# Performance work log

Hardware: AMD Instinct MI355X
Metric: run time of the kernel (lower is better)

Reference implementation:

```python
import jax, jax.numpy as jnp
import numpy as np

B, S, L, H, C = 16, 2048, 256, 768, 512

def setup_inputs() -> dict:
    key = jax.random.key(0)
    ks = jax.random.split(key, 9)
    sc = 1.0 / np.sqrt(H)
    return {
        "input_hidden_states": jax.random.normal(ks[0], (B, S, H), jnp.float32),
        "label_hidden_states": jax.random.normal(ks[1], (L, H), jnp.float32),
        "Wi": jax.random.normal(ks[2], (C, H), jnp.float32) * sc,
        "bi": jnp.zeros((C,), jnp.float32),
        "Wl": jax.random.normal(ks[3], (C, H), jnp.float32) * sc,
        "bl": jnp.zeros((C,), jnp.float32),
        "Wia": jax.random.normal(ks[4], (C, H), jnp.float32) * sc,
        "bia": jnp.zeros((C,), jnp.float32),
        "Wla": jax.random.normal(ks[5], (C, H), jnp.float32) * sc,
        "bla": jnp.zeros((C,), jnp.float32),
        "context": jax.random.uniform(ks[6], (C,), jnp.float32),
        "Wp": jax.random.normal(ks[7], (H, C), jnp.float32) * (1.0 / np.sqrt(C)),
    }

def reference(input_hidden_states, label_hidden_states, Wi, bi, Wl, bl,
              Wia, bia, Wla, bla, context, Wp):
    # Dropout is identity in eval mode.
    x = input_hidden_states            # [B,S,H]
    lab = label_hidden_states          # [L,H] (original repeats over batch; math is identical)
    input_trans = jax.nn.sigmoid(jnp.einsum('bsh,ch->bsc', x, Wi) + bi)      # [B,S,C]
    label_trans = jax.nn.sigmoid(lab @ Wl.T + bl)                            # [L,C]
    input_attn = jax.nn.sigmoid(jnp.einsum('bsh,ch->bsc', x, Wia) + bia)    # [B,S,C]
    label_attn = jax.nn.sigmoid(lab @ Wla.T + bla)                          # [L,C]
    # attn logits: (context * input_attn) @ label_attn^T  -> [B,S,L]
    logits = jnp.einsum('bsc,lc->bsl', input_attn * context, label_attn)
    attn = jax.nn.softmax(logits, axis=-1)                                   # [B,S,L]
    # trilinear reduction: sum_{s,l} input_trans[b,s,c] * attn[b,s,l] * label_trans[l,c]
    weighted = jnp.einsum('bsl,lc->bsc', attn, label_trans)                  # [B,S,C]
    fusion = jnp.sum(input_trans * weighted, axis=1)                         # [B,C]
    return fusion @ Wp.T                                                     # [B,H]
```

## Files before the change

### kernel.cpp

```cpp
#include <hip/hip_runtime.h>

#define H_DIM 768
#define C_DIM 512
#define L_DIM 256
#define S_DIM 2048
#define B_DIM 16

#define IA_STRIDE 520
#define ATTN_STRIDE 264
#define XP_STRIDE 776

typedef __attribute__((ext_vector_type(8))) short short8;
typedef __attribute__((ext_vector_type(4))) float f32x4;
typedef __attribute__((ext_vector_type(2))) __fp16 half2v;

#define MFMA_F16(a, b, c) __builtin_amdgcn_mfma_f32_16x16x32_f16((a), (b), (c), 0, 0, 0)

__device__ __forceinline__ unsigned short f2h(float f) {
    _Float16 h = (_Float16)f;
    return __builtin_bit_cast(unsigned short, h);
}
__device__ __forceinline__ float h2f(unsigned short u) {
    _Float16 h = __builtin_bit_cast(_Float16, u);
    return (float)h;
}
__device__ __forceinline__ float sigmoid_f(float x) { return 1.0f / (1.0f + __expf(-x)); }

__device__ __forceinline__ short8 cvt8(const float* p) {
    const float4* q = (const float4*)(const void*)p;
    float4 u = q[0], v = q[1];
    half2v h0 = __builtin_amdgcn_cvt_pkrtz(u.x, u.y);
    half2v h1 = __builtin_amdgcn_cvt_pkrtz(u.z, u.w);
    half2v h2 = __builtin_amdgcn_cvt_pkrtz(v.x, v.y);
    half2v h3 = __builtin_amdgcn_cvt_pkrtz(v.z, v.w);
    int4 pk = { __builtin_bit_cast(int, h0), __builtin_bit_cast(int, h1),
                __builtin_bit_cast(int, h2), __builtin_bit_cast(int, h3) };
    return __builtin_bit_cast(short8, pk);
}


__global__ __launch_bounds__(256) void prep_all(
    const float* __restrict__ x,
    const float* __restrict__ Wi, const float* __restrict__ Wia,
    const float* __restrict__ lab,
    const float* __restrict__ Wl,  const float* __restrict__ bl,
    const float* __restrict__ Wla, const float* __restrict__ bla,
    const float* __restrict__ ctx,
    unsigned short* __restrict__ x_f,
    unsigned short* __restrict__ Wi_f, unsigned short* __restrict__ Wia_f,
    unsigned short* __restrict__ la_f, unsigned short* __restrict__ lt_f,
    float* __restrict__ fusion)
{
    __shared__ unsigned short tile[16 * XP_STRIDE];
    const int t   = threadIdx.x;
    const int bid = blockIdx.x;

    if (bid == 0) {
        float4 z = {0.f, 0.f, 0.f, 0.f};
        float4* fp = (float4*)(void*)fusion;
#pragma unroll
        for (int i = 0; i < 8; ++i) fp[i * 256 + t] = z;
        return;
    }

    if (bid < 65) {
        const int lbid = bid - 1;
        const int wave = t >> 6;
        const int lane = t & 63;
        const int quad = lane >> 4;
        const int c16  = lane & 15;
        const int ct2  = lbid & 7;
        const int mh   = lbid >> 3;
        const int ct   = ct2 * 4 + wave;
        const int n0   = ct * 16;
        const int l0   = mh * 32;

        const f32x4 z4 = {0.f, 0.f, 0.f, 0.f};
        f32x4 a1[2], a2[2];
#pragma unroll
        for (int mt = 0; mt < 2; ++mt) { a1[mt] = z4; a2[mt] = z4; }

        const float* lb   = lab + (size_t)(l0 + c16) * H_DIM + quad * 8;
        const float* wlp  = Wl  + (size_t)(n0 + c16) * H_DIM + quad * 8;
        const float* wlap = Wla + (size_t)(n0 + c16) * H_DIM + quad * 8;
        for (int kt = 0; kt < 24; ++kt) {
            short8 b1 = cvt8(wlp + kt * 32);
            short8 b2 = cvt8(wlap + kt * 32);
#pragma unroll
            for (int mt = 0; mt < 2; ++mt) {
                short8 a = cvt8(lb + mt * 16 * H_DIM + kt * 32);
                a1[mt] = MFMA_F16(a, b1, a1[mt]);
                a2[mt] = MFMA_F16(a, b2, a2[mt]);
            }
        }
        const int c = n0 + c16;
        const float blv = bl[c], blav = bla[c], cv = ctx[c];
#pragma unroll
        for (int mt = 0; mt < 2; ++mt)
#pragma unroll
            for (int r = 0; r < 4; ++r) {
                const int l = l0 + mt * 16 + quad * 4 + r;
                const float ltv = sigmoid_f(a1[mt][r] + blv);
                const float lav = sigmoid_f(a2[mt][r] + blav) * cv;
                {
                    const int ctc = c >> 4, ktl = l >> 5;
                    const int frag = ((ctc >> 3) * 8 + ktl) * 8 + (ctc & 7);
                    const int ln = (c & 15) | (((l >> 3) & 3) << 4);
                    lt_f[((size_t)frag * 64 + ln) * 8 + (l & 7)] = f2h(ltv);
                }
                {
                    const int lt = l >> 4, ktc = c >> 5;
                    const int frag = ((lt >> 2) * 16 + ktc) * 4 + (lt & 3);
                    const int ln = (l & 15) | (((c >> 3) & 3) << 4);
                    la_f[((size_t)frag * 64 + ln) * 8 + (c & 7)] = f2h(lav);
                }
            }
        return;
    }

    if (bid < 449) {
        const int tid = (bid - 65) * 256 + t;
        const int m   = tid / 49152;
        const int idx = tid - m * 49152;
        const int ct   = idx / 1536;
        const int rem  = idx - ct * 1536;
        const int kt   = rem >> 6;
        const int lane = rem & 63;
        const int row  = ct * 16 + (lane & 15);
        const int kcol = kt * 32 + (lane >> 4) * 8;
        const float* src = (m == 0 ? Wi : Wia);
        unsigned short* dst = (m == 0 ? Wi_f : Wia_f);
        short8 v = cvt8(src + (size_t)row * H_DIM + kcol);
        const int frag = ((ct >> 3) * 24 + kt) * 8 + (ct & 7);
        *(short8*)(void*)(dst + ((size_t)frag * 64 + lane) * 8) = v;
        return;
    }

    {
        const int mt = bid - 449;
        const float4* src = (const float4*)(const void*)(x + (size_t)mt * 16 * H_DIM);
#pragma unroll
        for (int i = 0; i < 12; ++i) {
            const int id  = i * 256 + t;
            const int row = id / 192;
            const int c4  = id - row * 192;
            float4 v = src[id];
            half2v h0 = __builtin_amdgcn_cvt_pkrtz(v.x, v.y);
            half2v h1 = __builtin_amdgcn_cvt_pkrtz(v.z, v.w);
            uint2 pk = { __builtin_bit_cast(unsigned int, h0),
                         __builtin_bit_cast(unsigned int, h1) };
            *(uint2*)(void*)(tile + row * XP_STRIDE + c4 * 4) = pk;
        }
        __syncthreads();
        const int lane = t & 63;
        const int wave = t >> 6;
#pragma unroll
        for (int q = 0; q < 6; ++q) {
            const int kt = wave * 6 + q;
            short8 v = *(const short8*)(const void*)(
                tile + (lane & 15) * XP_STRIDE + kt * 32 + (lane >> 4) * 8);
            *(short8*)(void*)(x_f + ((size_t)(mt * 24 + kt) * 64 + lane) * 8) = v;
        }
    }
}

template<bool XF>
__global__ __launch_bounds__(512, 4) void fused_main(
    const unsigned short* __restrict__ x_f,
    const float* __restrict__ x,
    const float* __restrict__ bi,
    const float* __restrict__ bia,
    const unsigned short* __restrict__ Wi_f,
    const unsigned short* __restrict__ Wia_f,
    const unsigned short* __restrict__ lt_f,
    const unsigned short* __restrict__ la_f,
    float* __restrict__ fusion)
{
    __shared__ unsigned short lds_buf[64 * IA_STRIDE];
    __shared__ float rowscratch[8 * 64];
    __shared__ float inv_lds[64];

    const int tid  = threadIdx.x;
    const int wave = tid >> 6;
    const int lane = tid & 63;
    const int quad = lane >> 4;
    const int c16  = lane & 15;

    const int row0 = blockIdx.x * 64;
    const int b    = row0 >> 11;

    const f32x4 z4 = {0.f, 0.f, 0.f, 0.f};
    const int n0 = wave * 64;

    const float*  xb  = x + (size_t)(row0 + c16) * H_DIM + quad * 8;
    const short8* xf8 = (const short8*)(const void*)x_f + (size_t)blockIdx.x * 96 * 64 + lane;
    const size_t wofs = ((size_t)(wave >> 1) * 192 + (size_t)(wave & 1) * 4) * 64 + lane;

    {
        f32x4 acc[4][4];
#pragma unroll
        for (int m = 0; m < 4; ++m)
#pragma unroll
            for (int nt = 0; nt < 4; ++nt) acc[m][nt] = z4;
        const short8* wa8 = (const short8*)(const void*)Wia_f + wofs;
        for (int kt = 0; kt < 24; ++kt) {
            short8 a0, a1, a2, a3;
            if constexpr (XF) {
                a0 = xf8[kt * 64];        a1 = xf8[(24 + kt) * 64];
                a2 = xf8[(48 + kt) * 64]; a3 = xf8[(72 + kt) * 64];
            } else {
                a0 = cvt8(xb + kt * 32);                a1 = cvt8(xb + 16 * H_DIM + kt * 32);
                a2 = cvt8(xb + 32 * H_DIM + kt * 32);   a3 = cvt8(xb + 48 * H_DIM + kt * 32);
            }
#pragma unroll
            for (int nt = 0; nt < 4; ++nt) {
                short8 bw = wa8[(kt * 8 + nt) * 64];
                acc[0][nt] = MFMA_F16(a0, bw, acc[0][nt]);
                acc[1][nt] = MFMA_F16(a1, bw, acc[1][nt]);
                acc[2][nt] = MFMA_F16(a2, bw, acc[2][nt]);
                acc[3][nt] = MFMA_F16(a3, bw, acc[3][nt]);
            }
        }
#pragma unroll
        for (int nt = 0; nt < 4; ++nt) {
            const int col = n0 + nt * 16 + c16;
            const float bv = bia[col];
#pragma unroll
            for (int m = 0; m < 4; ++m)
#pragma unroll
                for (int r = 0; r < 4; ++r) {
                    const int row = m * 16 + quad * 4 + r;
                    lds_buf[row * IA_STRIDE + col] = f2h(sigmoid_f(acc[m][nt][r] + bv));
                }
        }
    }
    __syncthreads();

    const int n0l = wave * 32;
    f32x4 accl[4][2];
#pragma unroll
    for (int m = 0; m < 4; ++m)
#pragma unroll
        for (int j = 0; j < 2; ++j) accl[m][j] = z4;
    {
        const unsigned short* ab = lds_buf + c16 * IA_STRIDE + quad * 8;
        const short8* la8 = (const short8*)(const void*)la_f
                          + ((size_t)(wave >> 1) * 64 + (size_t)(wave & 1) * 2) * 64 + lane;
        for (int kt = 0; kt < 16; ++kt) {
            const int kk = kt * 32;
            short8 a0 = *(const short8*)(const void*)(ab + kk);
            short8 a1 = *(const short8*)(const void*)(ab + 16 * IA_STRIDE + kk);
            short8 a2 = *(const short8*)(const void*)(ab + 32 * IA_STRIDE + kk);
            short8 a3 = *(const short8*)(const void*)(ab + 48 * IA_STRIDE + kk);
#pragma unroll
            for (int j = 0; j < 2; ++j) {
                short8 bfr = la8[(kt * 4 + j) * 64];
                accl[0][j] = MFMA_F16(a0, bfr, accl[0][j]);
                accl[1][j] = MFMA_F16(a1, bfr, accl[1][j]);
                accl[2][j] = MFMA_F16(a2, bfr, accl[2][j]);
                accl[3][j] = MFMA_F16(a3, bfr, accl[3][j]);
            }
        }
    }
    __syncthreads();

    float rmax[4][4];
#pragma unroll
    for (int m = 0; m < 4; ++m)
#pragma unroll
        for (int r = 0; r < 4; ++r) {
            float mx = fmaxf(accl[m][0][r], accl[m][1][r]);
#pragma unroll
            for (int off = 1; off < 16; off <<= 1) mx = fmaxf(mx, __shfl_xor(mx, off, 64));
            rmax[m][r] = mx;
        }
    if (c16 == 0) {
#pragma unroll
        for (int m = 0; m < 4; ++m)
#pragma unroll
            for (int r = 0; r < 4; ++r)
                rowscratch[wave * 64 + m * 16 + quad * 4 + r] = rmax[m][r];
    }
    __syncthreads();
    float rsum[4][4];
#pragma unroll
    for (int m = 0; m < 4; ++m)
#pragma unroll
        for (int r = 0; r < 4; ++r) {
            const int row = m * 16 + quad * 4 + r;
            float gm = rowscratch[row];
#pragma unroll
            for (int w = 1; w < 8; ++w) gm = fmaxf(gm, rowscratch[w * 64 + row]);
            float s = 0.f;
#pragma unroll
            for (int j = 0; j < 2; ++j) {
                float e = __expf(accl[m][j][r] - gm);
                accl[m][j][r] = e;
                s += e;
            }
#pragma unroll
            for (int off = 1; off < 16; off <<= 1) s += __shfl_xor(s, off, 64);
            rsum[m][r] = s;
        }
    __syncthreads();
    if (c16 == 0) {
#pragma unroll
        for (int m = 0; m < 4; ++m)
#pragma unroll
            for (int r = 0; r < 4; ++r)
                rowscratch[wave * 64 + m * 16 + quad * 4 + r] = rsum[m][r];
    }
    __syncthreads();
#pragma unroll
    for (int m = 0; m < 4; ++m)
#pragma unroll
        for (int r = 0; r < 4; ++r) {
            const int row = m * 16 + quad * 4 + r;
            float st = 0.f;
#pragma unroll
            for (int w = 0; w < 8; ++w) st += rowscratch[w * 64 + row];
            if (wave == 0 && c16 == 0) inv_lds[row] = 1.0f / st;
#pragma unroll
            for (int j = 0; j < 2; ++j)
                lds_buf[row * ATTN_STRIDE + n0l + j * 16 + c16] = f2h(accl[m][j][r]);
        }
    __syncthreads();

    f32x4 accw[4][4];
#pragma unroll
    for (int m = 0; m < 4; ++m)
#pragma unroll
        for (int nt = 0; nt < 4; ++nt) accw[m][nt] = z4;
    {
        const unsigned short* ab = lds_buf + c16 * ATTN_STRIDE + quad * 8;
        const short8* lt8 = (const short8*)(const void*)lt_f
                          + ((size_t)(wave >> 1) * 64 + (size_t)(wave & 1) * 4) * 64 + lane;
        for (int kt = 0; kt < 8; ++kt) {
            const int kk = kt * 32;
            short8 a0 = *(const short8*)(const void*)(ab + kk);
            short8 a1 = *(const short8*)(const void*)(ab + 16 * ATTN_STRIDE + kk);
            short8 a2 = *(const short8*)(const void*)(ab + 32 * ATTN_STRIDE + kk);
            short8 a3 = *(const short8*)(const void*)(ab + 48 * ATTN_STRIDE + kk);
#pragma unroll
            for (int nt = 0; nt < 4; ++nt) {
                short8 bfr = lt8[(kt * 8 + nt) * 64];
                accw[0][nt] = MFMA_F16(a0, bfr, accw[0][nt]);
                accw[1][nt] = MFMA_F16(a1, bfr, accw[1][nt]);
                accw[2][nt] = MFMA_F16(a2, bfr, accw[2][nt]);
                accw[3][nt] = MFMA_F16(a3, bfr, accw[3][nt]);
            }
        }
    }
    __syncthreads();

    {
        float invr[4][4];
#pragma unroll
        for (int m = 0; m < 4; ++m)
#pragma unroll
            for (int r = 0; r < 4; ++r) invr[m][r] = inv_lds[m * 16 + quad * 4 + r];
#pragma unroll
        for (int nt = 0; nt < 4; ++nt) {
            const int col = n0 + nt * 16 + c16;
#pragma unroll
            for (int m = 0; m < 4; ++m)
#pragma unroll
                for (int r = 0; r < 4; ++r) {
                    const int row = m * 16 + quad * 4 + r;
                    lds_buf[row * IA_STRIDE + col] = f2h(accw[m][nt][r] * invr[m][r]);
                }
        }
    }

    {
        f32x4 acc[4][4];
#pragma unroll
        for (int m = 0; m < 4; ++m)
#pragma unroll
            for (int nt = 0; nt < 4; ++nt) acc[m][nt] = z4;
        const short8* wi8 = (const short8*)(const void*)Wi_f + wofs;
        for (int kt = 0; kt < 24; ++kt) {
            short8 a0, a1, a2, a3;
            if constexpr (XF) {
                a0 = xf8[kt * 64];        a1 = xf8[(24 + kt) * 64];
                a2 = xf8[(48 + kt) * 64]; a3 = xf8[(72 + kt) * 64];
            } else {
                a0 = cvt8(xb + kt * 32);                a1 = cvt8(xb + 16 * H_DIM + kt * 32);
                a2 = cvt8(xb + 32 * H_DIM + kt * 32);   a3 = cvt8(xb + 48 * H_DIM + kt * 32);
            }
#pragma unroll
            for (int nt = 0; nt < 4; ++nt) {
                short8 bw = wi8[(kt * 8 + nt) * 64];
                acc[0][nt] = MFMA_F16(a0, bw, acc[0][nt]);
                acc[1][nt] = MFMA_F16(a1, bw, acc[1][nt]);
                acc[2][nt] = MFMA_F16(a2, bw, acc[2][nt]);
                acc[3][nt] = MFMA_F16(a3, bw, acc[3][nt]);
            }
        }
#pragma unroll
        for (int nt = 0; nt < 4; ++nt) {
            const int col = n0 + nt * 16 + c16;
            const float bv = bi[col];
            float s = 0.f;
#pragma unroll
            for (int m = 0; m < 4; ++m)
#pragma unroll
                for (int r = 0; r < 4; ++r) {
                    const int row = m * 16 + quad * 4 + r;
                    s += h2f(lds_buf[row * IA_STRIDE + col]) * sigmoid_f(acc[m][nt][r] + bv);
                }
            s += __shfl_xor(s, 16, 64);
            s += __shfl_xor(s, 32, 64);
            if (lane < 16) atomicAdd(&fusion[b * C_DIM + col], s);
        }
    }
}

__global__ __launch_bounds__(256) void out_kernel(
    const float* __restrict__ fusion,
    const float* __restrict__ Wp,
    float* __restrict__ out)
{
    const int idx = blockIdx.x * 256 + threadIdx.x;
    const int R   = idx >> 3;
    const int sub = idx & 7;
    const int bb  = R / H_DIM;
    const int h   = R - bb * H_DIM;
    const float* wp = Wp + (size_t)h * C_DIM;
    const float* f  = fusion + bb * C_DIM;
    float s = 0.f;
#pragma unroll
    for (int j = 0; j < 16; ++j) {
        const int c = j * 32 + sub * 4;
        float4 wv = *(const float4*)(const void*)(wp + c);
        float4 fv = *(const float4*)(const void*)(f + c);
        s += fv.x * wv.x + fv.y * wv.y + fv.z * wv.z + fv.w * wv.w;
    }
    s += __shfl_xor(s, 1, 64);
    s += __shfl_xor(s, 2, 64);
    s += __shfl_xor(s, 4, 64);
    if (sub == 0) out[R] = s;
}

extern "C" void kernel_launch(void* const* d_in, const int* in_sizes, int n_in,
                              void* d_out, int out_size, void* d_ws, size_t ws_size,
                              hipStream_t stream)
{
    const float* x    = (const float*)d_in[0];
    const float* lab  = (const float*)d_in[1];
    const float* Wi   = (const float*)d_in[2];
    const float* bi   = (const float*)d_in[3];
    const float* Wl   = (const float*)d_in[4];
    const float* bl   = (const float*)d_in[5];
    const float* Wia  = (const float*)d_in[6];
    const float* bia  = (const float*)d_in[7];
    const float* Wla  = (const float*)d_in[8];
    const float* bla  = (const float*)d_in[9];
    const float* ctx  = (const float*)d_in[10];
    const float* Wp   = (const float*)d_in[11];

    char* ws = (char*)d_ws;
    unsigned short* Wi_f  = (unsigned short*)(ws);
    unsigned short* Wia_f = (unsigned short*)(ws + 786432);
    unsigned short* la_f  = (unsigned short*)(ws + 3145728);
    unsigned short* lt_f  = (unsigned short*)(ws + 3407872);
    float* fusion         = (float*)(ws + 3670016);
    unsigned short* x_f   = (unsigned short*)(ws + 3702784);
    const size_t NEED_XF  = 3702784 + (size_t)32768 * 768 * 2;

    if (ws_size >= NEED_XF) {
        prep_all<<<2497, 256, 0, stream>>>(
            x, Wi, Wia, lab, Wl, bl, Wla, bla, ctx,
            x_f, Wi_f, Wia_f, la_f, lt_f, fusion);
        fused_main<true><<<(B_DIM * S_DIM) / 64, 512, 0, stream>>>(
            x_f, x, bi, bia, Wi_f, Wia_f, lt_f, la_f, fusion);
    } else {
        prep_all<<<449, 256, 0, stream>>>(
            x, Wi, Wia, lab, Wl, bl, Wla, bla, ctx,
            nullptr, Wi_f, Wia_f, la_f, lt_f, fusion);
        fused_main<false><<<(B_DIM * S_DIM) / 64, 512, 0, stream>>>(
            nullptr, x, bi, bia, Wi_f, Wia_f, lt_f, la_f, fusion);
    }
    out_kernel<<<384, 256, 0, stream>>>(fusion, Wp, (float*)d_out);
}
```

Before: 286.3 us.

## Split input GEMM column tiles into two passes and trim softmax barriers

The Wia and Wi projection GEMMs now run in two passes of two 16-column tiles each, instead of one pass of four. This halves the live accumulator registers per wave, which is meant to relieve register pressure and spilling under the 512x4 launch bounds. The cost is that the x A-fragments are loaded twice per GEMM. The softmax now writes the exponentials straight into LDS and uses separate scratch buffers for max and sum, removing two block-wide barriers, and only wave 0 computes the inverse row sums.

```diff
diff --git a/kernel.cpp b/kernel.cpp
--- a/kernel.cpp
+++ b/kernel.cpp
@@ -177,7 +177,8 @@
     float* __restrict__ fusion)
 {
     __shared__ unsigned short lds_buf[64 * IA_STRIDE];
-    __shared__ float rowscratch[8 * 64];
+    __shared__ float scratchA[8 * 64];
+    __shared__ float scratchB[8 * 64];
     __shared__ float inv_lds[64];
 
     const int tid  = threadIdx.x;
@@ -197,41 +198,44 @@
     const size_t wofs = ((size_t)(wave >> 1) * 192 + (size_t)(wave & 1) * 4) * 64 + lane;
 
     {
-        f32x4 acc[4][4];
-#pragma unroll
-        for (int m = 0; m < 4; ++m)
-#pragma unroll
-            for (int nt = 0; nt < 4; ++nt) acc[m][nt] = z4;
         const short8* wa8 = (const short8*)(const void*)Wia_f + wofs;
-        for (int kt = 0; kt < 24; ++kt) {
-            short8 a0, a1, a2, a3;
-            if constexpr (XF) {
-                a0 = xf8[kt * 64];        a1 = xf8[(24 + kt) * 64];
-                a2 = xf8[(48 + kt) * 64]; a3 = xf8[(72 + kt) * 64];
-            } else {
-                a0 = cvt8(xb + kt * 32);                a1 = cvt8(xb + 16 * H_DIM + kt * 32);
-                a2 = cvt8(xb + 32 * H_DIM + kt * 32);   a3 = cvt8(xb + 48 * H_DIM + kt * 32);
-            }
-#pragma unroll
-            for (int nt = 0; nt < 4; ++nt) {
-                short8 bw = wa8[(kt * 8 + nt) * 64];
-                acc[0][nt] = MFMA_F16(a0, bw, acc[0][nt]);
-                acc[1][nt] = MFMA_F16(a1, bw, acc[1][nt]);
-                acc[2][nt] = MFMA_F16(a2, bw, acc[2][nt]);
-                acc[3][nt] = MFMA_F16(a3, bw, acc[3][nt]);
-            }
-        }
-#pragma unroll
-        for (int nt = 0; nt < 4; ++nt) {
-            const int col = n0 + nt * 16 + c16;
-            const float bv = bia[col];
+#pragma unroll 1
+        for (int half = 0; half < 2; ++half) {
+            f32x4 acc[4][2];
 #pragma unroll
             for (int m = 0; m < 4; ++m)
 #pragma unroll
-                for (int r = 0; r < 4; ++r) {
-                    const int row = m * 16 + quad * 4 + r;
-                    lds_buf[row * IA_STRIDE + col] = f2h(sigmoid_f(acc[m][nt][r] + bv));
-                }
+                for (int j = 0; j < 2; ++j) acc[m][j] = z4;
+            for (int kt = 0; kt < 24; ++kt) {
+                short8 a0, a1, a2, a3;
+                if constexpr (XF) {
+                    a0 = xf8[kt * 64];        a1 = xf8[(24 + kt) * 64];
+                    a2 = xf8[(48 + kt) * 64]; a3 = xf8[(72 + kt) * 64];
+                } else {
+                    a0 = cvt8(xb + kt * 32);                a1 = cvt8(xb + 16 * H_DIM + kt * 32);
+                    a2 = cvt8(xb + 32 * H_DIM + kt * 32);   a3 = cvt8(xb + 48 * H_DIM + kt * 32);
+                }
+#pragma unroll
+                for (int j = 0; j < 2; ++j) {
+                    short8 bw = wa8[(kt * 8 + half * 2 + j) * 64];
+                    acc[0][j] = MFMA_F16(a0, bw, acc[0][j]);
+                    acc[1][j] = MFMA_F16(a1, bw, acc[1][j]);
+                    acc[2][j] = MFMA_F16(a2, bw, acc[2][j]);
+                    acc[3][j] = MFMA_F16(a3, bw, acc[3][j]);
+                }
+            }
+#pragma unroll
+            for (int j = 0; j < 2; ++j) {
+                const int col = n0 + (half * 2 + j) * 16 + c16;
+                const float bv = bia[col];
+#pragma unroll
+                for (int m = 0; m < 4; ++m)
+#pragma unroll
+                    for (int r = 0; r < 4; ++r) {
+                        const int row = m * 16 + quad * 4 + r;
+                        lds_buf[row * IA_STRIDE + col] = f2h(sigmoid_f(acc[m][j][r] + bv));
+                    }
+            }
         }
     }
     __syncthreads();
@@ -264,7 +268,6 @@
     }
     __syncthreads();
 
-    float rmax[4][4];
 #pragma unroll
     for (int m = 0; m < 4; ++m)
 #pragma unroll
@@ -272,59 +275,39 @@
             float mx = fmaxf(accl[m][0][r], accl[m][1][r]);
 #pragma unroll
             for (int off = 1; off < 16; off <<= 1) mx = fmaxf(mx, __shfl_xor(mx, off, 64));
-            rmax[m][r] = mx;
-        }
-    if (c16 == 0) {
-#pragma unroll
-        for (int m = 0; m < 4; ++m)
-#pragma unroll
-            for (int r = 0; r < 4; ++r)
-                rowscratch[wave * 64 + m * 16 + quad * 4 + r] = rmax[m][r];
-    }
+            if (c16 == 0) scratchA[wave * 64 + m * 16 + quad * 4 + r] = mx;
+        }
     __syncthreads();
-    float rsum[4][4];
 #pragma unroll
     for (int m = 0; m < 4; ++m)
 #pragma unroll
         for (int r = 0; r < 4; ++r) {
             const int row = m * 16 + quad * 4 + r;
-            float gm = rowscratch[row];
-#pragma unroll
-            for (int w = 1; w < 8; ++w) gm = fmaxf(gm, rowscratch[w * 64 + row]);
-            float s = 0.f;
-#pragma unroll
-            for (int j = 0; j < 2; ++j) {
-                float e = __expf(accl[m][j][r] - gm);
-                accl[m][j][r] = e;
-                s += e;
-            }
+            float gm = scratchA[row];
+#pragma unroll
+            for (int w = 1; w < 8; ++w) gm = fmaxf(gm, scratchA[w * 64 + row]);
+            const float e0 = __expf(accl[m][0][r] - gm);
+            const float e1 = __expf(accl[m][1][r] - gm);
+            lds_buf[row * ATTN_STRIDE + n0l + c16]      = f2h(e0);
+            lds_buf[row * ATTN_STRIDE + n0l + 16 + c16] = f2h(e1);
+            float s = e0 + e1;
 #pragma unroll
             for (int off = 1; off < 16; off <<= 1) s += __shfl_xor(s, off, 64);
-            rsum[m][r] = s;
+            if (c16 == 0) scratchB[wave * 64 + row] = s;
         }
     __syncthreads();
-    if (c16 == 0) {
+    if (wave == 0 && c16 == 0) {
 #pragma unroll
         for (int m = 0; m < 4; ++m)
 #pragma unroll
-            for (int r = 0; r < 4; ++r)
-                rowscratch[wave * 64 + m * 16 + quad * 4 + r] = rsum[m][r];
-    }
-    __syncthreads();
-#pragma unroll
-    for (int m = 0; m < 4; ++m)
-#pragma unroll
-        for (int r = 0; r < 4; ++r) {
-            const int row = m * 16 + quad * 4 + r;
-            float st = 0.f;
-#pragma unroll
-            for (int w = 0; w < 8; ++w) st += rowscratch[w * 64 + row];
-            if (wave == 0 && c16 == 0) inv_lds[row] = 1.0f / st;
-#pragma unroll
-            for (int j = 0; j < 2; ++j)
-                lds_buf[row * ATTN_STRIDE + n0l + j * 16 + c16] = f2h(accl[m][j][r]);
-        }
-    __syncthreads();
+            for (int r = 0; r < 4; ++r) {
+                const int row = m * 16 + quad * 4 + r;
+                float st = 0.f;
+#pragma unroll
+                for (int w = 0; w < 8; ++w) st += scratchB[w * 64 + row];
+                inv_lds[row] = 1.0f / st;
+            }
+    }
 
     f32x4 accw[4][4];
 #pragma unroll
@@ -373,45 +356,48 @@
     }
 
     {
-        f32x4 acc[4][4];
-#pragma unroll
-        for (int m = 0; m < 4; ++m)
-#pragma unroll
-            for (int nt = 0; nt < 4; ++nt) acc[m][nt] = z4;
         const short8* wi8 = (const short8*)(const void*)Wi_f + wofs;
-        for (int kt = 0; kt < 24; ++kt) {
-            short8 a0, a1, a2, a3;
-            if constexpr (XF) {
-                a0 = xf8[kt * 64];        a1 = xf8[(24 + kt) * 64];
-                a2 = xf8[(48 + kt) * 64]; a3 = xf8[(72 + kt) * 64];
-            } else {
-                a0 = cvt8(xb + kt * 32);                a1 = cvt8(xb + 16 * H_DIM + kt * 32);
-                a2 = cvt8(xb + 32 * H_DIM + kt * 32);   a3 = cvt8(xb + 48 * H_DIM + kt * 32);
-            }
-#pragma unroll
-            for (int nt = 0; nt < 4; ++nt) {
-                short8 bw = wi8[(kt * 8 + nt) * 64];
-                acc[0][nt] = MFMA_F16(a0, bw, acc[0][nt]);
-                acc[1][nt] = MFMA_F16(a1, bw, acc[1][nt]);
-                acc[2][nt] = MFMA_F16(a2, bw, acc[2][nt]);
-                acc[3][nt] = MFMA_F16(a3, bw, acc[3][nt]);
-            }
-        }
-#pragma unroll
-        for (int nt = 0; nt < 4; ++nt) {
-            const int col = n0 + nt * 16 + c16;
-            const float bv = bi[col];
-            float s = 0.f;
+#pragma unroll 1
+        for (int half = 0; half < 2; ++half) {
+            f32x4 acc[4][2];
 #pragma unroll
             for (int m = 0; m < 4; ++m)
 #pragma unroll
-                for (int r = 0; r < 4; ++r) {
-                    const int row = m * 16 + quad * 4 + r;
-                    s += h2f(lds_buf[row * IA_STRIDE + col]) * sigmoid_f(acc[m][nt][r] + bv);
-                }
-            s += __shfl_xor(s, 16, 64);
-            s += __shfl_xor(s, 32, 64);
-            if (lane < 16) atomicAdd(&fusion[b * C_DIM + col], s);
+                for (int j = 0; j < 2; ++j) acc[m][j] = z4;
+            for (int kt = 0; kt < 24; ++kt) {
+                short8 a0, a1, a2, a3;
+                if constexpr (XF) {
+                    a0 = xf8[kt * 64];        a1 = xf8[(24 + kt) * 64];
+                    a2 = xf8[(48 + kt) * 64]; a3 = xf8[(72 + kt) * 64];
+                } else {
+                    a0 = cvt8(xb + kt * 32);                a1 = cvt8(xb + 16 * H_DIM + kt * 32);
+                    a2 = cvt8(xb + 32 * H_DIM + kt * 32);   a3 = cvt8(xb + 48 * H_DIM + kt * 32);
+                }
+#pragma unroll
+                for (int j = 0; j < 2; ++j) {
+                    short8 bw = wi8[(kt * 8 + half * 2 + j) * 64];
+                    acc[0][j] = MFMA_F16(a0, bw, acc[0][j]);
+                    acc[1][j] = MFMA_F16(a1, bw, acc[1][j]);
+                    acc[2][j] = MFMA_F16(a2, bw, acc[2][j]);
+                    acc[3][j] = MFMA_F16(a3, bw, acc[3][j]);
+                }
+            }
+#pragma unroll
+            for (int j = 0; j < 2; ++j) {
+                const int col = n0 + (half * 2 + j) * 16 + c16;
+                const float bv = bi[col];
+                float s = 0.f;
+#pragma unroll
+                for (int m = 0; m < 4; ++m)
+#pragma unroll
+                    for (int r = 0; r < 4; ++r) {
+                        const int row = m * 16 + quad * 4 + r;
+                        s += h2f(lds_buf[row * IA_STRIDE + col]) * sigmoid_f(acc[m][j][r] + bv);
+                    }
+                s += __shfl_xor(s, 16, 64);
+                s += __shfl_xor(s, 32, 64);
+                if (lane < 16) atomicAdd(&fusion[b * C_DIM + col], s);
+            }
         }
     }
 }
```

New measurement: 296.0 us. 3.4% more time.
